# Kernel tuning notes

Measured on AMD Instinct MI355X. Metric: run time of the kernel, lower is better.

The kernel has to match this reference:

```python
import jax, jax.numpy as jnp
import numpy as np

HID = 100  # LSTM hidden size (fixed in module)


def _lstm_final(x, Wih, Whh, bih, bhh, reverse):
    # x: [N, T, Hin]; returns final hidden state [N, HID] (PyTorch gate order i,f,g,o)
    xs = jnp.flip(x, axis=1) if reverse else x
    pre = jnp.einsum('nth,gh->ntg', xs, Wih) + bih + bhh  # [N, T, 4*HID]
    N = x.shape[0]
    h0 = jnp.zeros((N, HID), x.dtype)
    c0 = jnp.zeros((N, HID), x.dtype)

    def step(carry, pt):
        h, c = carry
        g = pt + h @ Whh.T
        i, f, gg, o = jnp.split(g, 4, axis=-1)
        c = jax.nn.sigmoid(f) * c + jax.nn.sigmoid(i) * jnp.tanh(gg)
        h = jax.nn.sigmoid(o) * jnp.tanh(c)
        return (h, c), None

    (h, c), _ = jax.lax.scan(step, (h0, c0), jnp.swapaxes(pre, 0, 1))
    return h


def setup_inputs():
    key = jax.random.key(0)
    ks = jax.random.split(key, 16)
    H, B, S, NP, PL = 768, 40, 128, 100, 20
    w = lambda k, shape: jax.random.normal(k, shape, jnp.float32) * 0.02
    return {
        'bert_output': jax.random.normal(ks[0], (B, S, H), jnp.float32),
        'commonsense': jax.random.normal(ks[1], (B * NP, PL, H), jnp.float32),
        'attention_mask': jnp.ones((B, S), jnp.int32),
        'commonsense_mask': jnp.ones((B, NP), jnp.int32),
        'b_size': 8, 'num_cand': 5, 'num_path': NP, 'path_len': PL,
        'lstm_Wih_f': w(ks[2], (4 * HID, H)), 'lstm_Whh_f': w(ks[3], (4 * HID, HID)),
        'lstm_bih_f': jnp.zeros((4 * HID,), jnp.float32), 'lstm_bhh_f': jnp.zeros((4 * HID,), jnp.float32),
        'lstm_Wih_b': w(ks[4], (4 * HID, H)), 'lstm_Whh_b': w(ks[5], (4 * HID, HID)),
        'lstm_bih_b': jnp.zeros((4 * HID,), jnp.float32), 'lstm_bhh_b': jnp.zeros((4 * HID,), jnp.float32),
        'proj_W': w(ks[6], (H, 2 * HID)), 'proj_b': jnp.zeros((H,), jnp.float32),
        'W1_w': w(ks[7], (1, H)), 'W1_b': jnp.zeros((1,), jnp.float32),
        'W2_w': w(ks[8], (1, H)), 'W2_b': jnp.zeros((1,), jnp.float32),
        'W3': w(ks[9], (1, 1, H)),
        'attp_W': w(ks[10], (H, 4 * H)), 'attp_b': jnp.zeros((H,), jnp.float32),
        'ln_w': jnp.ones((H,), jnp.float32), 'ln_b': jnp.zeros((H,), jnp.float32),
    }


def reference(bert_output, commonsense, attention_mask, commonsense_mask,
              b_size, num_cand, num_path, path_len,
              lstm_Wih_f, lstm_Whh_f, lstm_bih_f, lstm_bhh_f,
              lstm_Wih_b, lstm_Whh_b, lstm_bih_b, lstm_bhh_b,
              proj_W, proj_b, W1_w, W1_b, W2_w, W2_b, W3,
              attp_W, attp_b, ln_w, ln_b):
    Bc = b_size * num_cand
    # bidirectional LSTM over commonsense paths; only final hidden states are used
    h_f = _lstm_final(commonsense, lstm_Wih_f, lstm_Whh_f, lstm_bih_f, lstm_bhh_f, False)
    h_b = _lstm_final(commonsense, lstm_Wih_b, lstm_Whh_b, lstm_bih_b, lstm_bhh_b, True)
    enc = jnp.concatenate([h_f, h_b], axis=-1)               # [Bc*NP, 200]
    cs = jax.nn.relu(enc @ proj_W.T + proj_b).reshape(Bc, num_path, -1)  # [B, P, H]
    # trilinear BiDAF-style scores
    part1 = bert_output @ W1_w.T + W1_b                      # [B, S, 1]
    part2 = (cs @ W2_w.T + W2_b).transpose(0, 2, 1)          # [B, 1, P]
    part3 = jnp.einsum('bsh,bph->bsp', W3 * bert_output, cs)  # [B, S, P]
    mask_cs = (1.0 - commonsense_mask.astype(jnp.float32)) * -10000.0
    mask_dqa = (1.0 - attention_mask.astype(jnp.float32)) * -10000.0
    total = part1 + part2 + part3 + mask_cs[:, None, :] + mask_dqa[:, :, None]
    cs_att = jax.nn.softmax(total, axis=-1)                  # over paths
    weight_cs = jnp.einsum('bsp,bph->bsh', cs_att, cs)
    ctx_att = jax.nn.softmax(total, axis=1)                  # over context tokens
    probs = jnp.einsum('bsp,btp->bst', cs_att, ctx_att)      # [B, S, S]
    weighted_context = jnp.einsum('bst,bth->bsh', probs, bert_output)
    cat = jnp.concatenate([bert_output, weight_cs, bert_output * weight_cs,
                           bert_output * weighted_context], axis=-1)
    x = jax.nn.relu(cat @ attp_W.T + attp_b) + bert_output
    u = x.mean(-1, keepdims=True)
    s = ((x - u) ** 2).mean(-1, keepdims=True)
    return ln_w * ((x - u) / jnp.sqrt(s + 1e-12)) + ln_b
```

## Files before the change

kernel.cpp:

```cpp
#include <hip/hip_runtime.h>


typedef unsigned short ushort_t;
typedef unsigned int u32;
typedef __attribute__((ext_vector_type(8))) short short8;
typedef __attribute__((ext_vector_type(4))) float f32x4;
typedef __attribute__((address_space(1))) const u32 gu32;
typedef __attribute__((address_space(3))) u32 lu32;

__device__ __forceinline__ ushort_t f2bf(float f) {
  u32 x = __builtin_bit_cast(u32, f);
  u32 r = (x + 0x7fffu + ((x >> 16) & 1u)) >> 16;
  return (ushort_t)r;
}
__device__ __forceinline__ float bflo(u32 u) { return __builtin_bit_cast(float, u << 16); }
__device__ __forceinline__ float bfhi(u32 u) { return __builtin_bit_cast(float, u & 0xffff0000u); }
__device__ __forceinline__ u32 cvtpk(float lo, float hi) {
  u32 r;
  asm("v_cvt_pk_bf16_f32 %0, %1, %2" : "=v"(r) : "v"(lo), "v"(hi));
  return r;
}

__device__ __forceinline__ float sigm(float x) { return 1.f / (1.f + __expf(-x)); }
__device__ __forceinline__ float tanh_f(float x) { return 1.f - 2.f / (__expf(2.f * x) + 1.f); }


__global__ void prep_weights(const float* __restrict__ Wih_f, const float* __restrict__ Wih_b,
                             const float* __restrict__ Whh_f, const float* __restrict__ Whh_b,
                             const float* __restrict__ bih_f, const float* __restrict__ bhh_f,
                             const float* __restrict__ bih_b, const float* __restrict__ bhh_b,
                             const float* __restrict__ projW, const float* __restrict__ attpW,
                             ushort_t* __restrict__ wihcat, ushort_t* __restrict__ whhcat,
                             float* __restrict__ biascat, ushort_t* __restrict__ projw_bf,
                             ushort_t* __restrict__ attpw_bf) {
  const int TOT = 614400 + 102400 + 800 + 196608 + 2359296;
  for (int idx = blockIdx.x * 256 + threadIdx.x; idx < TOT; idx += gridDim.x * 256) {
    if (idx < 614400) {
      int g = idx / 768, k = idx % 768;
      float v = g < 400 ? Wih_f[g * 768 + k] : Wih_b[(g - 400) * 768 + k];
      wihcat[idx] = f2bf(v);
    } else if (idx < 716800) {
      int e = idx - 614400; int g = e / 128, j = e % 128;
      float v = 0.f;
      if (j < 100) v = g < 400 ? Whh_f[g * 100 + j] : Whh_b[(g - 400) * 100 + j];
      whhcat[e] = f2bf(v);
    } else if (idx < 717600) {
      int g = idx - 716800;
      biascat[g] = g < 400 ? bih_f[g] + bhh_f[g] : bih_b[g - 400] + bhh_b[g - 400];
    } else if (idx < 914208) {
      int e = idx - 717600; int o = e / 256, j = e % 256;
      float v = 0.f;
      if (j < 100) v = projW[o * 200 + j];
      else if (j >= 128 && j < 228) v = projW[o * 200 + 100 + (j - 128)];
      projw_bf[e] = f2bf(v);
    } else {
      int e = idx - 914208;
      attpw_bf[e] = f2bf(attpW[e]);
    }
  }
}

__global__ __launch_bounds__(256) void prep_bert(const float* __restrict__ bert,
                                                 const float* __restrict__ W3,
                                                 ushort_t* __restrict__ bw3,
                                                 ushort_t* __restrict__ bT) {
  __shared__ ushort_t tl[64 * 130];
  int ht = blockIdx.x, b = blockIdx.y;
  int h0 = ht * 64, tid = threadIdx.x;
  for (int e = tid; e < 8192; e += 256) {
    int t = e >> 6, hh = e & 63;
    float v = bert[((size_t)b * 128 + t) * 768 + h0 + hh];
    bw3[((size_t)b * 128 + t) * 768 + h0 + hh] = f2bf(v * W3[h0 + hh]);
    tl[hh * 130 + t] = f2bf(v);
  }
  __syncthreads();
  for (int e = tid; e < 8192; e += 256) {
    int hh = e >> 7, t = e & 127;
    bT[((size_t)b * 768 + h0 + hh) * 128 + t] = tl[hh * 130 + t];
  }
}

__global__ __launch_bounds__(256) void csT_k(const ushort_t* __restrict__ csb,
                                             ushort_t* __restrict__ csT) {
  __shared__ ushort_t tl[64 * 130];
  int ht = blockIdx.x, b = blockIdx.y;
  int h0 = ht * 64, tid = threadIdx.x;
  for (int e = tid; e < 6400; e += 256) {
    int p = e >> 6, hh = e & 63;
    tl[hh * 130 + p] = csb[((size_t)b * 100 + p) * 768 + h0 + hh];
  }
  __syncthreads();
  for (int e = tid; e < 8192; e += 256) {
    int hh = e >> 7, p = e & 127;
    csT[((size_t)b * 768 + h0 + hh) * 128 + p] = (p < 100) ? tl[hh * 130 + p] : (ushort_t)0;
  }
}


__global__ __launch_bounds__(256) void gemm_pre_f(
    const float* __restrict__ X,
    const ushort_t* __restrict__ B,
    const float* __restrict__ bias,
    ushort_t* __restrict__ P)
{
  __shared__ __align__(16) float lsA[128 * 64];
  __shared__ __align__(16) ushort_t lsB[128 * 64];
  int bid = blockIdx.x;
  int xcd = bid & 7, slot = bid >> 3;
  int L = (xcd < 7) ? xcd * 547 + slot : 3829 + slot;
  int bm = L / 7, bn = L - bm * 7;
  int m0 = bm * 128, n0 = bn * 128;
  int tid = threadIdx.x, lane = tid & 63, w = tid >> 6;
  int wr = w >> 1, wc = w & 1;
  int l15 = lane & 15, lk = lane >> 4;
  f32x4 acc[4][4];
  #pragma unroll
  for (int i = 0; i < 4; ++i)
    #pragma unroll
    for (int j = 0; j < 4; ++j)
      #pragma unroll
      for (int r = 0; r < 4; ++r) acc[i][j][r] = 0.f;

  size_t abase[8];
  #pragma unroll
  for (int i = 0; i < 8; ++i) {
    int seg = w * 8 + i;
    int row = seg * 4 + (lane >> 4);
    int m = m0 + row;
    int t = m / 4000, sq = m - t * 4000;
    int lc = (lane & 15) ^ (row & 15);
    abase[i] = ((size_t)sq * 20 + t) * 768 + lc * 4;
  }
  int r_in = lane >> 3, pslot = lane & 7;

  for (int kt = 0; kt < 12; ++kt) {
    __syncthreads();
    #pragma unroll
    for (int i = 0; i < 8; ++i) {
      int seg = w * 8 + i;
      __builtin_amdgcn_global_load_lds(
          (gu32*)(X + abase[i] + kt * 64),
          (lu32*)((char*)lsA + seg * 1024), 16, 0, 0);
    }
    #pragma unroll
    for (int i = 0; i < 4; ++i) {
      int seg = w * 4 + i;
      int row = seg * 8 + r_in;
      int sl = pslot ^ (row & 7);
      int n = n0 + row;
      if (n < 800)
        __builtin_amdgcn_global_load_lds(
            (gu32*)(B + (size_t)n * 768 + kt * 64 + sl * 8),
            (lu32*)(lsB + seg * 512), 16, 0, 0);
    }
    __syncthreads();
    #pragma unroll
    for (int ks = 0; ks < 2; ++ks) {
      short8 af[4], bfv[4];
      #pragma unroll
      for (int f = 0; f < 4; ++f) {
        int row = wr * 64 + f * 16 + l15;
        int c0 = ks * 8 + lk * 2;
        int pc0 = c0 ^ (row & 15), pc1 = (c0 + 1) ^ (row & 15);
        float4 v0 = *reinterpret_cast<const float4*>(&lsA[row * 64 + pc0 * 4]);
        float4 v1 = *reinterpret_cast<const float4*>(&lsA[row * 64 + pc1 * 4]);
        int4 pk;
        pk.x = (int)cvtpk(v0.x, v0.y);
        pk.y = (int)cvtpk(v0.z, v0.w);
        pk.z = (int)cvtpk(v1.x, v1.y);
        pk.w = (int)cvtpk(v1.z, v1.w);
        af[f] = __builtin_bit_cast(short8, pk);
        int rowb = wc * 64 + f * 16 + l15;
        bfv[f] = *reinterpret_cast<const short8*>(
            &lsB[rowb * 64 + (((ks * 4 + lk) ^ (rowb & 7)) << 3)]);
      }
      #pragma unroll
      for (int fm = 0; fm < 4; ++fm)
        #pragma unroll
        for (int fn = 0; fn < 4; ++fn)
          acc[fm][fn] = __builtin_amdgcn_mfma_f32_16x16x32_bf16(af[fm], bfv[fn], acc[fm][fn], 0, 0, 0);
    }
  }
  #pragma unroll
  for (int fm = 0; fm < 4; ++fm) {
    int mb = m0 + wr * 64 + fm * 16;
    int t = mb / 4000;
    int sq = mb - t * 4000;
    int cch = sq >> 4;
    #pragma unroll
    for (int fn = 0; fn < 4; ++fn) {
      int nb = n0 + wc * 64 + fn * 16;
      if (nb < 800) {
        int nl = nb < 400 ? nb : nb - 400;
        int nq = (nb < 400 ? 0 : 25) + (nl >> 4);
        float bsv = bias[nb + l15];
        uint2 pk;
        pk.x = cvtpk(acc[fm][fn][0] + bsv, acc[fm][fn][1] + bsv);
        pk.y = cvtpk(acc[fm][fn][2] + bsv, acc[fm][fn][3] + bsv);
        *reinterpret_cast<uint2*>(
            &P[((((size_t)t * 250 + cch) * 50 + nq) << 8) + l15 * 16 + lk * 4]) = pk;
      }
    }
  }
}


template <int EPI>
__global__ __launch_bounds__(256) void gemm128(
    const ushort_t* __restrict__ A, int lda,
    const ushort_t* __restrict__ B, int ldb,
    int M, int N, int KT,
    const float* __restrict__ bias,
    const float* __restrict__ resid,
    float* __restrict__ C, int ldc,
    ushort_t* __restrict__ C2,
    int nbn, int swq, int swr)
{
  __shared__ __align__(16) ushort_t lsA[128 * 64];
  __shared__ __align__(16) ushort_t lsB[128 * 64];
  int bm, bn;
  if (nbn > 0) {
    int bid = blockIdx.x, xcd = bid & 7, slot = bid >> 3;
    int L = (xcd < swr) ? xcd * (swq + 1) + slot
                        : swr * (swq + 1) + (xcd - swr) * swq + slot;
    bm = L / nbn; bn = L - bm * nbn;
  } else {
    bm = blockIdx.x; bn = blockIdx.y;
  }
  int m0 = bm * 128, n0 = bn * 128;
  int tid = threadIdx.x, lane = tid & 63, w = tid >> 6;
  int wr = w >> 1, wc = w & 1;
  int l15 = lane & 15, lk = lane >> 4;
  f32x4 acc[4][4];
  #pragma unroll
  for (int i = 0; i < 4; ++i)
    #pragma unroll
    for (int j = 0; j < 4; ++j)
      #pragma unroll
      for (int r = 0; r < 4; ++r) acc[i][j][r] = 0.f;

  int r_in = lane >> 3, p = lane & 7;
  for (int kt = 0; kt < KT; ++kt) {
    __syncthreads();
    #pragma unroll
    for (int i = 0; i < 4; ++i) {
      int seg = w * 4 + i;
      int row = seg * 8 + r_in;
      int sl = p ^ (row & 7);
      int m = m0 + row;
      if (m < M)
        __builtin_amdgcn_global_load_lds(
            (gu32*)(A + (size_t)m * lda + kt * 64 + sl * 8),
            (lu32*)(lsA + seg * 512), 16, 0, 0);
      int n = n0 + row;
      if (n < N)
        __builtin_amdgcn_global_load_lds(
            (gu32*)(B + (size_t)n * ldb + kt * 64 + sl * 8),
            (lu32*)(lsB + seg * 512), 16, 0, 0);
    }
    __syncthreads();
    #pragma unroll
    for (int ks = 0; ks < 2; ++ks) {
      short8 af[4], bfv[4];
      #pragma unroll
      for (int f = 0; f < 4; ++f) {
        int row = wr * 64 + f * 16 + l15;
        af[f] = *reinterpret_cast<const short8*>(
            &lsA[row * 64 + (((ks * 4 + lk) ^ (row & 7)) << 3)]);
        int rowb = wc * 64 + f * 16 + l15;
        bfv[f] = *reinterpret_cast<const short8*>(
            &lsB[rowb * 64 + (((ks * 4 + lk) ^ (rowb & 7)) << 3)]);
      }
      #pragma unroll
      for (int fm = 0; fm < 4; ++fm)
        #pragma unroll
        for (int fn = 0; fn < 4; ++fn)
          acc[fm][fn] = __builtin_amdgcn_mfma_f32_16x16x32_bf16(af[fm], bfv[fn], acc[fm][fn], 0, 0, 0);
    }
  }
  #pragma unroll
  for (int fm = 0; fm < 4; ++fm)
    #pragma unroll
    for (int fn = 0; fn < 4; ++fn)
      #pragma unroll
      for (int r = 0; r < 4; ++r) {
        int m = m0 + wr * 64 + fm * 16 + lk * 4 + r;
        int n = n0 + wc * 64 + fn * 16 + l15;
        if (m < M && n < N) {
          float v = acc[fm][fn][r] + bias[n];
          v = fmaxf(v, 0.f);
          if (EPI == 2) v += resid[(size_t)m * ldc + n];
          C[(size_t)m * ldc + n] = v;
          if (EPI == 1 && C2) C2[(size_t)m * ldc + n] = f2bf(v);
        }
      }
}


template <int EPI>
__global__ __launch_bounds__(256) void gemm128b(
    const ushort_t* __restrict__ A, long long sA, int lda,
    const ushort_t* __restrict__ Bm, long long sB, int ldb,
    int M, int N, int KT,
    float* __restrict__ Cf, ushort_t* __restrict__ Cb, long long sC, int ldc,
    const float* __restrict__ p1, const float* __restrict__ p2,
    const int* __restrict__ am, const int* __restrict__ cm)
{
  __shared__ __align__(16) ushort_t lsA[128 * 64];
  __shared__ __align__(16) ushort_t lsB[128 * 64];
  int b = blockIdx.z;
  const ushort_t* Ab = A + (size_t)b * sA;
  const ushort_t* Bb = Bm + (size_t)b * sB;
  int n0 = blockIdx.x * 128;
  int tid = threadIdx.x, lane = tid & 63, w = tid >> 6;
  int wr = w >> 1, wc = w & 1;
  int l15 = lane & 15, lk = lane >> 4;
  f32x4 acc[4][4];
  #pragma unroll
  for (int i = 0; i < 4; ++i)
    #pragma unroll
    for (int j = 0; j < 4; ++j)
      #pragma unroll
      for (int r = 0; r < 4; ++r) acc[i][j][r] = 0.f;

  int r_in = lane >> 3, p = lane & 7;
  for (int kt = 0; kt < KT; ++kt) {
    __syncthreads();
    #pragma unroll
    for (int i = 0; i < 4; ++i) {
      int seg = w * 4 + i;
      int row = seg * 8 + r_in;
      int sl = p ^ (row & 7);
      if (row < M)
        __builtin_amdgcn_global_load_lds(
            (gu32*)(Ab + (size_t)row * lda + kt * 64 + sl * 8),
            (lu32*)(lsA + seg * 512), 16, 0, 0);
      int n = n0 + row;
      if (n < N)
        __builtin_amdgcn_global_load_lds(
            (gu32*)(Bb + (size_t)n * ldb + kt * 64 + sl * 8),
            (lu32*)(lsB + seg * 512), 16, 0, 0);
    }
    __syncthreads();
    #pragma unroll
    for (int ks = 0; ks < 2; ++ks) {
      short8 af[4], bfv[4];
      #pragma unroll
      for (int f = 0; f < 4; ++f) {
        int row = wr * 64 + f * 16 + l15;
        af[f] = *reinterpret_cast<const short8*>(
            &lsA[row * 64 + (((ks * 4 + lk) ^ (row & 7)) << 3)]);
        int rowb = wc * 64 + f * 16 + l15;
        bfv[f] = *reinterpret_cast<const short8*>(
            &lsB[rowb * 64 + (((ks * 4 + lk) ^ (rowb & 7)) << 3)]);
      }
      #pragma unroll
      for (int fm = 0; fm < 4; ++fm)
        #pragma unroll
        for (int fn = 0; fn < 4; ++fn)
          acc[fm][fn] = __builtin_amdgcn_mfma_f32_16x16x32_bf16(af[fm], bfv[fn], acc[fm][fn], 0, 0, 0);
    }
  }
  #pragma unroll
  for (int fm = 0; fm < 4; ++fm)
    #pragma unroll
    for (int fn = 0; fn < 4; ++fn)
      #pragma unroll
      for (int r = 0; r < 4; ++r) {
        int m = wr * 64 + fm * 16 + lk * 4 + r;
        int n = n0 + wc * 64 + fn * 16 + l15;
        if (m < M && n < N) {
          float v = acc[fm][fn][r];
          if (EPI == 10) {
            v += p1[b * M + m] + p2[b * N + n];
            v += (1.f - (float)am[b * M + m]) * -10000.f;
            v += (1.f - (float)cm[b * N + n]) * -10000.f;
            Cf[(size_t)b * sC + (size_t)m * ldc + n] = v;
          } else {
            Cb[(size_t)b * sC + (size_t)m * ldc + n] = f2bf(v);
          }
        }
      }
}


__global__ __launch_bounds__(256) void lstm_recur(
    const ushort_t* __restrict__ pre,
    const ushort_t* __restrict__ whh,
    ushort_t* __restrict__ hcat)
{
  __shared__ __align__(16) ushort_t gx[25 * 256];
  __shared__ __align__(16) ushort_t h_lds[16 * 128];

  int dir = blockIdx.y;
  int c = blockIdx.x;
  int tid = threadIdx.x, lane = tid & 63, w = tid >> 6;
  int s = lane & 15, lk = lane >> 4;

  short8 wf[7][4];
  #pragma unroll
  for (int qi = 0; qi < 7; ++qi) {
    int q = w + qi * 4;
    if (q < 25) {
      const ushort_t* wp = whh + ((size_t)dir * 400 + q * 16 + s) * 128;
      #pragma unroll
      for (int ks = 0; ks < 4; ++ks)
        wf[qi][ks] = *reinterpret_cast<const short8*>(wp + ks * 32 + lk * 8);
    }
  }
  for (int e = tid; e < 1024; e += 256)
    *reinterpret_cast<u32*>(&h_lds[e * 2]) = 0u;

  float cst[2][4];
  #pragma unroll
  for (int g = 0; g < 2; ++g)
    #pragma unroll
    for (int r = 0; r < 4; ++r) cst[g][r] = 0.f;

  uint2 pvA[7], pvB[7];
  {
    int tt0 = dir ? 19 : 0;
    const ushort_t* pb = pre + ((((size_t)tt0 * 250 + c) * 50 + dir * 25) << 8);
    #pragma unroll
    for (int qi = 0; qi < 7; ++qi) {
      int q = w + qi * 4;
      if (q < 25) pvA[qi] = *reinterpret_cast<const uint2*>(pb + (q << 8) + s * 16 + lk * 4);
    }
  }
  __syncthreads();

  auto step = [&](uint2 (&pvc)[7], uint2 (&pvn)[7], int t) {
    f32x4 acc[7];
    #pragma unroll
    for (int qi = 0; qi < 7; ++qi)
      #pragma unroll
      for (int r = 0; r < 4; ++r) acc[qi][r] = 0.f;
    #pragma unroll
    for (int ks = 0; ks < 4; ++ks) {
      short8 af = *reinterpret_cast<const short8*>(
          &h_lds[s * 128 + (((ks * 4 + lk) ^ s) << 3)]);
      #pragma unroll
      for (int qi = 0; qi < 7; ++qi)
        if (w + qi * 4 < 25)
          acc[qi] = __builtin_amdgcn_mfma_f32_16x16x32_bf16(af, wf[qi][ks], acc[qi], 0, 0, 0);
    }
    #pragma unroll
    for (int qi = 0; qi < 7; ++qi)
      if (w + qi * 4 < 25) {
        acc[qi][0] += bflo(pvc[qi].x); acc[qi][1] += bfhi(pvc[qi].x);
        acc[qi][2] += bflo(pvc[qi].y); acc[qi][3] += bfhi(pvc[qi].y);
      }
    if (t + 1 < 20) {
      int tn = dir ? 19 - (t + 1) : (t + 1);
      const ushort_t* pb = pre + ((((size_t)tn * 250 + c) * 50 + dir * 25) << 8);
      #pragma unroll
      for (int qi = 0; qi < 7; ++qi) {
        int q = w + qi * 4;
        if (q < 25) pvn[qi] = *reinterpret_cast<const uint2*>(pb + (q << 8) + s * 16 + lk * 4);
      }
    }
    #pragma unroll
    for (int qi = 0; qi < 7; ++qi) {
      int q = w + qi * 4;
      if (q < 25) {
        ushort4 pk;
        pk.x = f2bf(acc[qi][0]); pk.y = f2bf(acc[qi][1]);
        pk.z = f2bf(acc[qi][2]); pk.w = f2bf(acc[qi][3]);
        *reinterpret_cast<ushort4*>(&gx[(q << 8) + s * 16 + lk * 4]) = pk;
      }
    }
    __syncthreads();
    #pragma unroll
    for (int gd = 0; gd < 2; ++gd) {
      int gi = w + gd * 4;
      if (gi < 7) {
        int j = gi * 16 + s;
        if (j < 100) {
          auto ld2 = [&](int q, int sp) {
            return *reinterpret_cast<const uint2*>(&gx[(q << 8) + sp * 16 + lk * 4]);
          };
          uint2 iv = ld2(gi, s);
          uint2 fv = (s < 12) ? ld2(6 + gi, s + 4) : ld2(7 + gi, s - 12);
          uint2 gv = (s < 8) ? ld2(12 + gi, s + 8) : ld2(13 + gi, s - 8);
          uint2 ov = (s < 4) ? ld2(18 + gi, s + 12) : ld2(19 + gi, s - 4);
          float ia[4] = {bflo(iv.x), bfhi(iv.x), bflo(iv.y), bfhi(iv.y)};
          float fa[4] = {bflo(fv.x), bfhi(fv.x), bflo(fv.y), bfhi(fv.y)};
          float ga[4] = {bflo(gv.x), bfhi(gv.x), bflo(gv.y), bfhi(gv.y)};
          float oa[4] = {bflo(ov.x), bfhi(ov.x), bflo(ov.y), bfhi(ov.y)};
          #pragma unroll
          for (int r = 0; r < 4; ++r) {
            float cc = sigm(fa[r]) * cst[gd][r] + sigm(ia[r]) * tanh_f(ga[r]);
            cst[gd][r] = cc;
            int row = lk * 4 + r;
            h_lds[row * 128 + (((j >> 3) ^ row) << 3) + (j & 7)] =
                f2bf(sigm(oa[r]) * tanh_f(cc));
          }
        }
      }
    }
    __syncthreads();
  };

  #pragma unroll 1
  for (int tp = 0; tp < 10; ++tp) {
    step(pvA, pvB, 2 * tp);
    step(pvB, pvA, 2 * tp + 1);
  }

  {
    int row = tid >> 4, sl = tid & 15;
    uint2 v = *reinterpret_cast<const uint2*>(&h_lds[row * 128 + ((sl ^ row) << 3)]);
    *reinterpret_cast<uint2*>(&hcat[(size_t)(c * 16 + row) * 256 + dir * 128 + sl * 8]) = v;
  }
}


__global__ void rowdot2(const float* __restrict__ bert, const float* __restrict__ cs,
                        const float* __restrict__ W1w, const float* __restrict__ W1b,
                        const float* __restrict__ W2w, const float* __restrict__ W2b,
                        float* __restrict__ part1, float* __restrict__ part2) {
  int row = blockIdx.x;
  int lane = threadIdx.x;
  const float* x;
  const float* wv;
  float b0;
  float* out;
  if (row < 5120) { x = bert + (size_t)row * 768; wv = W1w; b0 = W1b[0]; out = part1 + row; }
  else { int r = row - 5120; x = cs + (size_t)r * 768; wv = W2w; b0 = W2b[0]; out = part2 + r; }
  float s = 0.f;
  for (int k = lane; k < 768; k += 64) s += x[k] * wv[k];
  for (int off = 32; off; off >>= 1) s += __shfl_down(s, off);
  if (lane == 0) *out = s + b0;
}

__global__ void softmax_both(const float* __restrict__ total,
                             ushort_t* __restrict__ csatt,
                             ushort_t* __restrict__ ctxatt) {
  int bid = blockIdx.x;
  int lane = threadIdx.x;
  if (bid < 5120) {
    const float* x = total + (size_t)bid * 100;
    float e0 = x[lane];
    bool has1 = (lane + 64) < 100;
    float e1 = has1 ? x[lane + 64] : -3.4e38f;
    float m = fmaxf(e0, e1);
    for (int off = 32; off; off >>= 1) m = fmaxf(m, __shfl_xor(m, off));
    float s0 = expf(e0 - m), s1 = has1 ? expf(e1 - m) : 0.f;
    float s = s0 + s1;
    for (int off = 32; off; off >>= 1) s += __shfl_xor(s, off);
    float inv = 1.f / s;
    csatt[(size_t)bid * 128 + lane] = f2bf(s0 * inv);
    csatt[(size_t)bid * 128 + lane + 64] = has1 ? f2bf(s1 * inv) : (ushort_t)0;
  } else {
    int idx = bid - 5120;
    int b = idx / 100, p = idx - b * 100;
    const float* base = total + (size_t)b * 12800 + p;
    float e0 = base[lane * 100], e1 = base[(lane + 64) * 100];
    float m = fmaxf(e0, e1);
    for (int off = 32; off; off >>= 1) m = fmaxf(m, __shfl_xor(m, off));
    float s0 = expf(e0 - m), s1 = expf(e1 - m);
    float s = s0 + s1;
    for (int off = 32; off; off >>= 1) s += __shfl_xor(s, off);
    float inv = 1.f / s;
    ctxatt[((size_t)b * 128 + lane) * 128 + p] = f2bf(s0 * inv);
    ctxatt[((size_t)b * 128 + lane + 64) * 128 + p] = f2bf(s1 * inv);
  }
}

__global__ void catk(const float* __restrict__ bert, const ushort_t* __restrict__ wcs,
                     const ushort_t* __restrict__ wctx, ushort_t* __restrict__ cat) {
  const int TOT = 5120 * 192;
  for (int i = blockIdx.x * 256 + threadIdx.x; i < TOT; i += gridDim.x * 256) {
    int row = i / 192, h4 = i - row * 192;
    size_t e = (size_t)row * 768 + h4 * 4;
    float4 bv = *reinterpret_cast<const float4*>(bert + e);
    ushort4 wv = *reinterpret_cast<const ushort4*>(wcs + e);
    ushort4 cv = *reinterpret_cast<const ushort4*>(wctx + e);
    ushort_t* out = cat + (size_t)row * 3072 + h4 * 4;
    ushort4 s0, s2, s3;
    s0.x = f2bf(bv.x); s0.y = f2bf(bv.y); s0.z = f2bf(bv.z); s0.w = f2bf(bv.w);
    s2.x = f2bf(bv.x * bflo((u32)wv.x)); s2.y = f2bf(bv.y * bflo((u32)wv.y));
    s2.z = f2bf(bv.z * bflo((u32)wv.z)); s2.w = f2bf(bv.w * bflo((u32)wv.w));
    s3.x = f2bf(bv.x * bflo((u32)cv.x)); s3.y = f2bf(bv.y * bflo((u32)cv.y));
    s3.z = f2bf(bv.z * bflo((u32)cv.z)); s3.w = f2bf(bv.w * bflo((u32)cv.w));
    *reinterpret_cast<ushort4*>(out) = s0;
    *reinterpret_cast<ushort4*>(out + 768) = wv;
    *reinterpret_cast<ushort4*>(out + 1536) = s2;
    *reinterpret_cast<ushort4*>(out + 2304) = s3;
  }
}

__global__ __launch_bounds__(256) void layernorm(float* __restrict__ X,
                                                 const float* __restrict__ w,
                                                 const float* __restrict__ bta) {
  int row = blockIdx.x;
  float* x = X + (size_t)row * 768;
  int t = threadIdx.x;
  float v[3];
  float s = 0.f;
  #pragma unroll
  for (int i = 0; i < 3; ++i) { v[i] = x[t + 256 * i]; s += v[i]; }
  __shared__ float red[256];
  red[t] = s; __syncthreads();
  for (int off = 128; off; off >>= 1) { if (t < off) red[t] += red[t + off]; __syncthreads(); }
  float mean = red[0] * (1.f / 768.f);
  __syncthreads();
  float q = 0.f;
  #pragma unroll
  for (int i = 0; i < 3; ++i) { float d = v[i] - mean; q += d * d; }
  red[t] = q; __syncthreads();
  for (int off = 128; off; off >>= 1) { if (t < off) red[t] += red[t + off]; __syncthreads(); }
  float inv = rsqrtf(red[0] * (1.f / 768.f) + 1e-12f);
  #pragma unroll
  for (int i = 0; i < 3; ++i) {
    int k = t + 256 * i;
    x[k] = w[k] * ((v[i] - mean) * inv) + bta[k];
  }
}


extern "C" void kernel_launch(void* const* d_in, const int* in_sizes, int n_in,
                              void* d_out, int out_size, void* d_ws, size_t ws_size,
                              hipStream_t stream) {
  (void)in_sizes; (void)n_in; (void)out_size; (void)ws_size;
  const float* bert  = (const float*)d_in[0];
  const float* cmn   = (const float*)d_in[1];
  const int*   amask = (const int*)d_in[2];
  const int*   cmask = (const int*)d_in[3];
  const float* Wih_f = (const float*)d_in[8];
  const float* Whh_f = (const float*)d_in[9];
  const float* bih_f = (const float*)d_in[10];
  const float* bhh_f = (const float*)d_in[11];
  const float* Wih_b = (const float*)d_in[12];
  const float* Whh_b = (const float*)d_in[13];
  const float* bih_b = (const float*)d_in[14];
  const float* bhh_b = (const float*)d_in[15];
  const float* projW = (const float*)d_in[16];
  const float* projb = (const float*)d_in[17];
  const float* W1w   = (const float*)d_in[18];
  const float* W1b   = (const float*)d_in[19];
  const float* W2w   = (const float*)d_in[20];
  const float* W2b   = (const float*)d_in[21];
  const float* W3    = (const float*)d_in[22];
  const float* attpW = (const float*)d_in[23];
  const float* attpb = (const float*)d_in[24];
  const float* lnw   = (const float*)d_in[25];
  const float* lnb   = (const float*)d_in[26];

  char* base = (char*)d_ws;
  size_t off = 0;
  auto alloc = [&](size_t bytes) -> char* {
    char* r = base + off;
    off += (bytes + 255) & ~(size_t)255;
    return r;
  };
  ushort_t* wihcat   = (ushort_t*)alloc(800 * 768 * 2);
  ushort_t* whhcat   = (ushort_t*)alloc(800 * 128 * 2);
  float*    biascat  = (float*)alloc(800 * 4);
  ushort_t* projw_bf = (ushort_t*)alloc(768 * 256 * 2);
  ushort_t* attpw_bf = (ushort_t*)alloc(768 * 3072 * 2);
  ushort_t* hcat     = (ushort_t*)alloc(4000 * 256 * 2);
  float*    cs       = (float*)alloc((size_t)4000 * 768 * 4);
  ushort_t* cs_bf    = (ushort_t*)alloc((size_t)4000 * 768 * 2);
  ushort_t* csT      = (ushort_t*)alloc((size_t)40 * 768 * 128 * 2);
  float*    part1    = (float*)alloc(5120 * 4);
  float*    part2    = (float*)alloc(4000 * 4);
  float*    total_s  = (float*)alloc((size_t)40 * 128 * 100 * 4);
  ushort_t* csatt_bf = (ushort_t*)alloc((size_t)40 * 128 * 128 * 2);
  ushort_t* ctxatt_bf= (ushort_t*)alloc((size_t)40 * 128 * 128 * 2);
  ushort_t* probs_bf = (ushort_t*)alloc((size_t)40 * 128 * 128 * 2);
  ushort_t* wcs_bf   = (ushort_t*)alloc((size_t)40 * 128 * 768 * 2);
  ushort_t* wctx_bf  = (ushort_t*)alloc((size_t)40 * 128 * 768 * 2);
  ushort_t* bw3_bf   = (ushort_t*)alloc((size_t)40 * 128 * 768 * 2);
  ushort_t* bertT    = (ushort_t*)alloc((size_t)40 * 768 * 128 * 2);
  ushort_t* cat      = (ushort_t*)alloc((size_t)5120 * 3072 * 2);
  ushort_t* pre      = (ushort_t*)alloc((size_t)20 * 250 * 50 * 256 * 2);

  prep_weights<<<512, 256, 0, stream>>>(Wih_f, Wih_b, Whh_f, Whh_b, bih_f, bhh_f, bih_b, bhh_b,
                                        projW, attpW, wihcat, whhcat, biascat, projw_bf, attpw_bf);
  prep_bert<<<dim3(12, 40), 256, 0, stream>>>(bert, W3, bw3_bf, bertT);

  gemm_pre_f<<<4375, 256, 0, stream>>>(cmn, wihcat, biascat, pre);
  lstm_recur<<<dim3(250, 2), 256, 0, stream>>>(pre, whhcat, hcat);

  gemm128<1><<<dim3(32, 6), 256, 0, stream>>>(hcat, 256, projw_bf, 256, 4000, 768, 4,
                                              projb, nullptr, cs, 768, cs_bf, 0, 0, 0);
  csT_k<<<dim3(12, 40), 256, 0, stream>>>(cs_bf, csT);
  rowdot2<<<9120, 64, 0, stream>>>(bert, cs, W1w, W1b, W2w, W2b, part1, part2);

  gemm128b<10><<<dim3(1, 1, 40), 256, 0, stream>>>(
      bw3_bf, 98304LL, 768, cs_bf, 76800LL, 768, 128, 100, 12,
      total_s, nullptr, 12800LL, 100, part1, part2, amask, cmask);
  softmax_both<<<9120, 64, 0, stream>>>(total_s, csatt_bf, ctxatt_bf);
  gemm128b<11><<<dim3(6, 1, 40), 256, 0, stream>>>(
      csatt_bf, 16384LL, 128, csT, 98304LL, 128, 128, 768, 2,
      nullptr, wcs_bf, 98304LL, 768, nullptr, nullptr, nullptr, nullptr);
  gemm128b<11><<<dim3(1, 1, 40), 256, 0, stream>>>(
      csatt_bf, 16384LL, 128, ctxatt_bf, 16384LL, 128, 128, 128, 2,
      nullptr, probs_bf, 16384LL, 128, nullptr, nullptr, nullptr, nullptr);
  gemm128b<11><<<dim3(6, 1, 40), 256, 0, stream>>>(
      probs_bf, 16384LL, 128, bertT, 98304LL, 128, 128, 768, 2,
      nullptr, wctx_bf, 98304LL, 768, nullptr, nullptr, nullptr, nullptr);

  catk<<<2048, 256, 0, stream>>>(bert, wcs_bf, wctx_bf, cat);
  gemm128<2><<<240, 256, 0, stream>>>(cat, 3072, attpw_bf, 3072, 5120, 768, 48,
                                      attpb, bert, (float*)d_out, 768, nullptr, 6, 30, 0);
  layernorm<<<5120, 256, 0, stream>>>((float*)d_out, lnw, lnb);
}
```

Measured before the change: 535.4 us.

## Fuse attention GEMMs and concat epilogues, pre-convert LSTM input, retile GEMMs

The commonsense input is now converted to bf16 in time-major order by a separate kernel, so the input-projection GEMM reads bf16 through a 128x160 tile instead of converting fp32 in its inner loop. The score GEMM is split four ways along K, and the mask and part1/part2 additions move into the softmax, which sums the four partials. The cs-weighted and probs GEMMs are merged by placing the context-attention matrix next to csT, and their epilogues write straight into the concat buffer, so catk and two intermediate buffers go away. The final projection uses 64-row tiles to launch more blocks. The costs are an extra full pass writing bf16 x, and redundant partial-sum traffic in the softmax.

```diff
diff --git a/kernel.cpp b/kernel.cpp
--- a/kernel.cpp
+++ b/kernel.cpp
@@ -60,18 +60,34 @@
   }
 }
 
+__global__ void convert_x_t(const float4* __restrict__ x4, ushort_t* __restrict__ xb) {
+  for (int i = blockIdx.x * 256 + threadIdx.x; i < 15360000; i += gridDim.x * 256) {
+    int seq = i / 3840;
+    int rem = i - seq * 3840;
+    int t = rem / 192;
+    int k4 = rem - t * 192;
+    float4 v = x4[i];
+    ushort4 o;
+    o.x = f2bf(v.x); o.y = f2bf(v.y); o.z = f2bf(v.z); o.w = f2bf(v.w);
+    *reinterpret_cast<ushort4*>(&xb[((size_t)t * 4000 + seq) * 768 + k4 * 4]) = o;
+  }
+}
+
 __global__ __launch_bounds__(256) void prep_bert(const float* __restrict__ bert,
                                                  const float* __restrict__ W3,
                                                  ushort_t* __restrict__ bw3,
-                                                 ushort_t* __restrict__ bT) {
+                                                 ushort_t* __restrict__ bT,
+                                                 ushort_t* __restrict__ cat) {
   __shared__ ushort_t tl[64 * 130];
   int ht = blockIdx.x, b = blockIdx.y;
   int h0 = ht * 64, tid = threadIdx.x;
   for (int e = tid; e < 8192; e += 256) {
     int t = e >> 6, hh = e & 63;
     float v = bert[((size_t)b * 128 + t) * 768 + h0 + hh];
+    ushort_t vb = f2bf(v);
     bw3[((size_t)b * 128 + t) * 768 + h0 + hh] = f2bf(v * W3[h0 + hh]);
-    tl[hh * 130 + t] = f2bf(v);
+    cat[((size_t)b * 128 + t) * 3072 + h0 + hh] = vb;
+    tl[hh * 130 + t] = vb;
   }
   __syncthreads();
   for (int e = tid; e < 8192; e += 256) {
@@ -81,7 +97,7 @@
 }
 
 __global__ __launch_bounds__(256) void csT_k(const ushort_t* __restrict__ csb,
-                                             ushort_t* __restrict__ csT) {
+                                             ushort_t* __restrict__ csTcat) {
   __shared__ ushort_t tl[64 * 130];
   int ht = blockIdx.x, b = blockIdx.y;
   int h0 = ht * 64, tid = threadIdx.x;
@@ -92,92 +108,76 @@
   __syncthreads();
   for (int e = tid; e < 8192; e += 256) {
     int hh = e >> 7, p = e & 127;
-    csT[((size_t)b * 768 + h0 + hh) * 128 + p] = (p < 100) ? tl[hh * 130 + p] : (ushort_t)0;
-  }
-}
-
-
-__global__ __launch_bounds__(256) void gemm_pre_f(
-    const float* __restrict__ X,
+    csTcat[((size_t)b * 896 + h0 + hh) * 128 + p] = (p < 100) ? tl[hh * 130 + p] : (ushort_t)0;
+  }
+}
+
+
+__global__ __launch_bounds__(256) void gemm_pre160(
+    const ushort_t* __restrict__ A,
     const ushort_t* __restrict__ B,
     const float* __restrict__ bias,
     ushort_t* __restrict__ P)
 {
-  __shared__ __align__(16) float lsA[128 * 64];
-  __shared__ __align__(16) ushort_t lsB[128 * 64];
+  __shared__ __align__(16) ushort_t lsA[128 * 64];
+  __shared__ __align__(16) ushort_t lsB[160 * 64];
   int bid = blockIdx.x;
   int xcd = bid & 7, slot = bid >> 3;
-  int L = (xcd < 7) ? xcd * 547 + slot : 3829 + slot;
-  int bm = L / 7, bn = L - bm * 7;
-  int m0 = bm * 128, n0 = bn * 128;
+  int L = (xcd < 5) ? xcd * 391 + slot : 1955 + (xcd - 5) * 390 + slot;
+  int bm = L / 5, bn = L - bm * 5;
+  int m0 = bm * 128, n0 = bn * 160;
   int tid = threadIdx.x, lane = tid & 63, w = tid >> 6;
   int wr = w >> 1, wc = w & 1;
   int l15 = lane & 15, lk = lane >> 4;
-  f32x4 acc[4][4];
+  f32x4 acc[4][5];
   #pragma unroll
   for (int i = 0; i < 4; ++i)
     #pragma unroll
-    for (int j = 0; j < 4; ++j)
+    for (int j = 0; j < 5; ++j)
       #pragma unroll
       for (int r = 0; r < 4; ++r) acc[i][j][r] = 0.f;
 
-  size_t abase[8];
-  #pragma unroll
-  for (int i = 0; i < 8; ++i) {
-    int seg = w * 8 + i;
-    int row = seg * 4 + (lane >> 4);
-    int m = m0 + row;
-    int t = m / 4000, sq = m - t * 4000;
-    int lc = (lane & 15) ^ (row & 15);
-    abase[i] = ((size_t)sq * 20 + t) * 768 + lc * 4;
-  }
-  int r_in = lane >> 3, pslot = lane & 7;
-
+  int r_in = lane >> 3, p = lane & 7;
   for (int kt = 0; kt < 12; ++kt) {
     __syncthreads();
-    #pragma unroll
-    for (int i = 0; i < 8; ++i) {
-      int seg = w * 8 + i;
-      __builtin_amdgcn_global_load_lds(
-          (gu32*)(X + abase[i] + kt * 64),
-          (lu32*)((char*)lsA + seg * 1024), 16, 0, 0);
-    }
     #pragma unroll
     for (int i = 0; i < 4; ++i) {
       int seg = w * 4 + i;
       int row = seg * 8 + r_in;
-      int sl = pslot ^ (row & 7);
-      int n = n0 + row;
-      if (n < 800)
-        __builtin_amdgcn_global_load_lds(
-            (gu32*)(B + (size_t)n * 768 + kt * 64 + sl * 8),
-            (lu32*)(lsB + seg * 512), 16, 0, 0);
+      int sl = p ^ (row & 7);
+      __builtin_amdgcn_global_load_lds(
+          (gu32*)(A + (size_t)(m0 + row) * 768 + kt * 64 + sl * 8),
+          (lu32*)(lsA + seg * 512), 16, 0, 0);
+    }
+    #pragma unroll
+    for (int i = 0; i < 5; ++i) {
+      int seg = w * 5 + i;
+      int row = seg * 8 + r_in;
+      int sl = p ^ (row & 7);
+      __builtin_amdgcn_global_load_lds(
+          (gu32*)(B + (size_t)(n0 + row) * 768 + kt * 64 + sl * 8),
+          (lu32*)(lsB + seg * 512), 16, 0, 0);
     }
     __syncthreads();
     #pragma unroll
     for (int ks = 0; ks < 2; ++ks) {
-      short8 af[4], bfv[4];
+      short8 af[4], bfv[5];
       #pragma unroll
       for (int f = 0; f < 4; ++f) {
         int row = wr * 64 + f * 16 + l15;
-        int c0 = ks * 8 + lk * 2;
-        int pc0 = c0 ^ (row & 15), pc1 = (c0 + 1) ^ (row & 15);
-        float4 v0 = *reinterpret_cast<const float4*>(&lsA[row * 64 + pc0 * 4]);
-        float4 v1 = *reinterpret_cast<const float4*>(&lsA[row * 64 + pc1 * 4]);
-        int4 pk;
-        pk.x = (int)cvtpk(v0.x, v0.y);
-        pk.y = (int)cvtpk(v0.z, v0.w);
-        pk.z = (int)cvtpk(v1.x, v1.y);
-        pk.w = (int)cvtpk(v1.z, v1.w);
-        af[f] = __builtin_bit_cast(short8, pk);
-        int rowb = wc * 64 + f * 16 + l15;
+        af[f] = *reinterpret_cast<const short8*>(
+            &lsA[row * 64 + (((ks * 4 + lk) ^ (row & 7)) << 3)]);
+      }
+      #pragma unroll
+      for (int f = 0; f < 5; ++f) {
+        int rowb = wc * 80 + f * 16 + l15;
         bfv[f] = *reinterpret_cast<const short8*>(
             &lsB[rowb * 64 + (((ks * 4 + lk) ^ (rowb & 7)) << 3)]);
       }
       #pragma unroll
       for (int fm = 0; fm < 4; ++fm)
         #pragma unroll
-        for (int fn = 0; fn < 4; ++fn)
+        for (int fn = 0; fn < 5; ++fn)
           acc[fm][fn] = __builtin_amdgcn_mfma_f32_16x16x32_bf16(af[fm], bfv[fn], acc[fm][fn], 0, 0, 0);
     }
   }
@@ -188,45 +188,32 @@
     int sq = mb - t * 4000;
     int cch = sq >> 4;
     #pragma unroll
-    for (int fn = 0; fn < 4; ++fn) {
-      int nb = n0 + wc * 64 + fn * 16;
-      if (nb < 800) {
-        int nl = nb < 400 ? nb : nb - 400;
-        int nq = (nb < 400 ? 0 : 25) + (nl >> 4);
-        float bsv = bias[nb + l15];
-        uint2 pk;
-        pk.x = cvtpk(acc[fm][fn][0] + bsv, acc[fm][fn][1] + bsv);
-        pk.y = cvtpk(acc[fm][fn][2] + bsv, acc[fm][fn][3] + bsv);
-        *reinterpret_cast<uint2*>(
-            &P[((((size_t)t * 250 + cch) * 50 + nq) << 8) + l15 * 16 + lk * 4]) = pk;
-      }
-    }
-  }
-}
-
-
-template <int EPI>
-__global__ __launch_bounds__(256) void gemm128(
+    for (int fn = 0; fn < 5; ++fn) {
+      int nb = n0 + wc * 80 + fn * 16;
+      int nl = nb < 400 ? nb : nb - 400;
+      int nq = (nb < 400 ? 0 : 25) + (nl >> 4);
+      float bsv = bias[nb + l15];
+      uint2 pk;
+      pk.x = cvtpk(acc[fm][fn][0] + bsv, acc[fm][fn][1] + bsv);
+      pk.y = cvtpk(acc[fm][fn][2] + bsv, acc[fm][fn][3] + bsv);
+      *reinterpret_cast<uint2*>(
+          &P[((((size_t)t * 250 + cch) * 50 + nq) << 8) + l15 * 16 + lk * 4]) = pk;
+    }
+  }
+}
+
+
+__global__ __launch_bounds__(256) void gemm_proj(
     const ushort_t* __restrict__ A, int lda,
     const ushort_t* __restrict__ B, int ldb,
     int M, int N, int KT,
     const float* __restrict__ bias,
-    const float* __restrict__ resid,
     float* __restrict__ C, int ldc,
-    ushort_t* __restrict__ C2,
-    int nbn, int swq, int swr)
+    ushort_t* __restrict__ C2)
 {
   __shared__ __align__(16) ushort_t lsA[128 * 64];
   __shared__ __align__(16) ushort_t lsB[128 * 64];
-  int bm, bn;
-  if (nbn > 0) {
-    int bid = blockIdx.x, xcd = bid & 7, slot = bid >> 3;
-    int L = (xcd < swr) ? xcd * (swq + 1) + slot
-                        : swr * (swq + 1) + (xcd - swr) * swq + slot;
-    bm = L / nbn; bn = L - bm * nbn;
-  } else {
-    bm = blockIdx.x; bn = blockIdx.y;
-  }
+  int bm = blockIdx.x, bn = blockIdx.y;
   int m0 = bm * 128, n0 = bn * 128;
   int tid = threadIdx.x, lane = tid & 63, w = tid >> 6;
   int wr = w >> 1, wc = w & 1;
@@ -287,11 +274,9 @@
         int m = m0 + wr * 64 + fm * 16 + lk * 4 + r;
         int n = n0 + wc * 64 + fn * 16 + l15;
         if (m < M && n < N) {
-          float v = acc[fm][fn][r] + bias[n];
-          v = fmaxf(v, 0.f);
-          if (EPI == 2) v += resid[(size_t)m * ldc + n];
+          float v = fmaxf(acc[fm][fn][r] + bias[n], 0.f);
           C[(size_t)m * ldc + n] = v;
-          if (EPI == 1 && C2) C2[(size_t)m * ldc + n] = f2bf(v);
+          C2[(size_t)m * ldc + n] = f2bf(v);
         }
       }
 }
@@ -302,13 +287,13 @@
     const ushort_t* __restrict__ A, long long sA, int lda,
     const ushort_t* __restrict__ Bm, long long sB, int ldb,
     int M, int N, int KT,
-    float* __restrict__ Cf, ushort_t* __restrict__ Cb, long long sC, int ldc,
-    const float* __restrict__ p1, const float* __restrict__ p2,
-    const int* __restrict__ am, const int* __restrict__ cm)
+    float* __restrict__ Cf, ushort_t* __restrict__ Cb,
+    const float* __restrict__ bertp, ushort_t* __restrict__ catp)
 {
   __shared__ __align__(16) ushort_t lsA[128 * 64];
   __shared__ __align__(16) ushort_t lsB[128 * 64];
   int b = blockIdx.z;
+  int koff = blockIdx.y * KT * 64;
   const ushort_t* Ab = A + (size_t)b * sA;
   const ushort_t* Bb = Bm + (size_t)b * sB;
   int n0 = blockIdx.x * 128;
@@ -333,12 +318,12 @@
       int sl = p ^ (row & 7);
       if (row < M)
         __builtin_amdgcn_global_load_lds(
-            (gu32*)(Ab + (size_t)row * lda + kt * 64 + sl * 8),
+            (gu32*)(Ab + (size_t)row * lda + koff + kt * 64 + sl * 8),
             (lu32*)(lsA + seg * 512), 16, 0, 0);
       int n = n0 + row;
       if (n < N)
         __builtin_amdgcn_global_load_lds(
-            (gu32*)(Bb + (size_t)n * ldb + kt * 64 + sl * 8),
+            (gu32*)(Bb + (size_t)n * ldb + koff + kt * 64 + sl * 8),
             (lu32*)(lsB + seg * 512), 16, 0, 0);
     }
     __syncthreads();
@@ -372,14 +357,105 @@
         if (m < M && n < N) {
           float v = acc[fm][fn][r];
           if (EPI == 10) {
-            v += p1[b * M + m] + p2[b * N + n];
-            v += (1.f - (float)am[b * M + m]) * -10000.f;
-            v += (1.f - (float)cm[b * N + n]) * -10000.f;
-            Cf[(size_t)b * sC + (size_t)m * ldc + n] = v;
+            Cf[(size_t)blockIdx.y * 512000 + (size_t)b * 12800 + (size_t)m * 100 + n] = v;
+          } else if (EPI == 12) {
+            size_t row3 = ((size_t)b * 128 + m) * 3072;
+            if (n < 768) {
+              float bv = bertp[((size_t)b * 128 + m) * 768 + n];
+              ushort_t wv = f2bf(v);
+              catp[row3 + 768 + n] = wv;
+              catp[row3 + 1536 + n] = f2bf(bv * bflo((u32)wv));
+            } else {
+              Cb[(size_t)b * 16384 + (size_t)m * 128 + (n - 768)] = f2bf(v);
+            }
           } else {
-            Cb[(size_t)b * sC + (size_t)m * ldc + n] = f2bf(v);
+            float bv = bertp[((size_t)b * 128 + m) * 768 + n];
+            catp[((size_t)b * 128 + m) * 3072 + 2304 + n] = f2bf(bv * v);
           }
         }
+      }
+}
+
+
+__global__ __launch_bounds__(256) void gemm64_attp(
+    const ushort_t* __restrict__ A,
+    const ushort_t* __restrict__ B,
+    const float* __restrict__ bias,
+    const float* __restrict__ resid,
+    float* __restrict__ C)
+{
+  __shared__ __align__(16) ushort_t lsA[64 * 64];
+  __shared__ __align__(16) ushort_t lsB[128 * 64];
+  int bid = blockIdx.x;
+  int xcd = bid & 7, slot = bid >> 3;
+  int L = xcd * 60 + slot;
+  int bm = L / 6, bn = L - bm * 6;
+  int m0 = bm * 64, n0 = bn * 128;
+  int tid = threadIdx.x, lane = tid & 63, w = tid >> 6;
+  int wr = w >> 1, wc = w & 1;
+  int l15 = lane & 15, lk = lane >> 4;
+  f32x4 acc[2][4];
+  #pragma unroll
+  for (int i = 0; i < 2; ++i)
+    #pragma unroll
+    for (int j = 0; j < 4; ++j)
+      #pragma unroll
+      for (int r = 0; r < 4; ++r) acc[i][j][r] = 0.f;
+
+  int r_in = lane >> 3, p = lane & 7;
+  for (int kt = 0; kt < 48; ++kt) {
+    __syncthreads();
+    #pragma unroll
+    for (int i = 0; i < 2; ++i) {
+      int seg = w * 2 + i;
+      int row = seg * 8 + r_in;
+      int sl = p ^ (row & 7);
+      __builtin_amdgcn_global_load_lds(
+          (gu32*)(A + (size_t)(m0 + row) * 3072 + kt * 64 + sl * 8),
+          (lu32*)(lsA + seg * 512), 16, 0, 0);
+    }
+    #pragma unroll
+    for (int i = 0; i < 4; ++i) {
+      int seg = w * 4 + i;
+      int row = seg * 8 + r_in;
+      int sl = p ^ (row & 7);
+      __builtin_amdgcn_global_load_lds(
+          (gu32*)(B + (size_t)(n0 + row) * 3072 + kt * 64 + sl * 8),
+          (lu32*)(lsB + seg * 512), 16, 0, 0);
+    }
+    __syncthreads();
+    #pragma unroll
+    for (int ks = 0; ks < 2; ++ks) {
+      short8 af[2], bfv[4];
+      #pragma unroll
+      for (int f = 0; f < 2; ++f) {
+        int row = wr * 32 + f * 16 + l15;
+        af[f] = *reinterpret_cast<const short8*>(
+            &lsA[row * 64 + (((ks * 4 + lk) ^ (row & 7)) << 3)]);
+      }
+      #pragma unroll
+      for (int f = 0; f < 4; ++f) {
+        int rowb = wc * 64 + f * 16 + l15;
+        bfv[f] = *reinterpret_cast<const short8*>(
+            &lsB[rowb * 64 + (((ks * 4 + lk) ^ (rowb & 7)) << 3)]);
+      }
+      #pragma unroll
+      for (int fm = 0; fm < 2; ++fm)
+        #pragma unroll
+        for (int fn = 0; fn < 4; ++fn)
+          acc[fm][fn] = __builtin_amdgcn_mfma_f32_16x16x32_bf16(af[fm], bfv[fn], acc[fm][fn], 0, 0, 0);
+    }
+  }
+  #pragma unroll
+  for (int fm = 0; fm < 2; ++fm)
+    #pragma unroll
+    for (int fn = 0; fn < 4; ++fn)
+      #pragma unroll
+      for (int r = 0; r < 4; ++r) {
+        int m = m0 + wr * 32 + fm * 16 + lk * 4 + r;
+        int n = n0 + wc * 64 + fn * 16 + l15;
+        float v = fmaxf(acc[fm][fn][r] + bias[n], 0.f) + resid[(size_t)m * 768 + n];
+        C[(size_t)m * 768 + n] = v;
       }
 }
 
@@ -533,16 +609,28 @@
   if (lane == 0) *out = s + b0;
 }
 
-__global__ void softmax_both(const float* __restrict__ total,
+__global__ void softmax_both(const float* __restrict__ t4,
+                             const float* __restrict__ part1,
+                             const float* __restrict__ part2,
+                             const int* __restrict__ amask,
+                             const int* __restrict__ cmask,
                              ushort_t* __restrict__ csatt,
-                             ushort_t* __restrict__ ctxatt) {
+                             ushort_t* __restrict__ csTcat) {
   int bid = blockIdx.x;
   int lane = threadIdx.x;
+  auto tsum = [&](size_t idx) {
+    return t4[idx] + t4[idx + 512000] + t4[idx + 1024000] + t4[idx + 1536000];
+  };
   if (bid < 5120) {
-    const float* x = total + (size_t)bid * 100;
-    float e0 = x[lane];
+    int b = bid >> 7;
+    size_t base = (size_t)bid * 100;
+    float e0 = tsum(base + lane) + part2[b * 100 + lane]
+               + (1.f - (float)cmask[b * 100 + lane]) * -10000.f;
     bool has1 = (lane + 64) < 100;
-    float e1 = has1 ? x[lane + 64] : -3.4e38f;
+    float e1 = -3.4e38f;
+    if (has1)
+      e1 = tsum(base + lane + 64) + part2[b * 100 + lane + 64]
+           + (1.f - (float)cmask[b * 100 + lane + 64]) * -10000.f;
     float m = fmaxf(e0, e1);
     for (int off = 32; off; off >>= 1) m = fmaxf(m, __shfl_xor(m, off));
     float s0 = expf(e0 - m), s1 = has1 ? expf(e1 - m) : 0.f;
@@ -554,39 +642,20 @@
   } else {
     int idx = bid - 5120;
     int b = idx / 100, p = idx - b * 100;
-    const float* base = total + (size_t)b * 12800 + p;
-    float e0 = base[lane * 100], e1 = base[(lane + 64) * 100];
+    size_t base = (size_t)b * 12800 + p;
+    int t0 = lane, t1 = lane + 64;
+    float e0 = tsum(base + (size_t)t0 * 100) + part1[b * 128 + t0]
+               + (1.f - (float)amask[b * 128 + t0]) * -10000.f;
+    float e1 = tsum(base + (size_t)t1 * 100) + part1[b * 128 + t1]
+               + (1.f - (float)amask[b * 128 + t1]) * -10000.f;
     float m = fmaxf(e0, e1);
     for (int off = 32; off; off >>= 1) m = fmaxf(m, __shfl_xor(m, off));
     float s0 = expf(e0 - m), s1 = expf(e1 - m);
     float s = s0 + s1;
     for (int off = 32; off; off >>= 1) s += __shfl_xor(s, off);
     float inv = 1.f / s;
-    ctxatt[((size_t)b * 128 + lane) * 128 + p] = f2bf(s0 * inv);
-    ctxatt[((size_t)b * 128 + lane + 64) * 128 + p] = f2bf(s1 * inv);
-  }
-}
-
-__global__ void catk(const float* __restrict__ bert, const ushort_t* __restrict__ wcs,
-                     const ushort_t* __restrict__ wctx, ushort_t* __restrict__ cat) {
-  const int TOT = 5120 * 192;
-  for (int i = blockIdx.x * 256 + threadIdx.x; i < TOT; i += gridDim.x * 256) {
-    int row = i / 192, h4 = i - row * 192;
-    size_t e = (size_t)row * 768 + h4 * 4;
-    float4 bv = *reinterpret_cast<const float4*>(bert + e);
-    ushort4 wv = *reinterpret_cast<const ushort4*>(wcs + e);
-    ushort4 cv = *reinterpret_cast<const ushort4*>(wctx + e);
-    ushort_t* out = cat + (size_t)row * 3072 + h4 * 4;
-    ushort4 s0, s2, s3;
-    s0.x = f2bf(bv.x); s0.y = f2bf(bv.y); s0.z = f2bf(bv.z); s0.w = f2bf(bv.w);
-    s2.x = f2bf(bv.x * bflo((u32)wv.x)); s2.y = f2bf(bv.y * bflo((u32)wv.y));
-    s2.z = f2bf(bv.z * bflo((u32)wv.z)); s2.w = f2bf(bv.w * bflo((u32)wv.w));
-    s3.x = f2bf(bv.x * bflo((u32)cv.x)); s3.y = f2bf(bv.y * bflo((u32)cv.y));
-    s3.z = f2bf(bv.z * bflo((u32)cv.z)); s3.w = f2bf(bv.w * bflo((u32)cv.w));
-    *reinterpret_cast<ushort4*>(out) = s0;
-    *reinterpret_cast<ushort4*>(out + 768) = wv;
-    *reinterpret_cast<ushort4*>(out + 1536) = s2;
-    *reinterpret_cast<ushort4*>(out + 2304) = s3;
+    csTcat[((size_t)b * 896 + 768 + t0) * 128 + p] = f2bf(s0 * inv);
+    csTcat[((size_t)b * 896 + 768 + t1) * 128 + p] = f2bf(s1 * inv);
   }
 }
 
@@ -662,48 +731,43 @@
   ushort_t* hcat     = (ushort_t*)alloc(4000 * 256 * 2);
   float*    cs       = (float*)alloc((size_t)4000 * 768 * 4);
   ushort_t* cs_bf    = (ushort_t*)alloc((size_t)4000 * 768 * 2);
-  ushort_t* csT      = (ushort_t*)alloc((size_t)40 * 768 * 128 * 2);
+  ushort_t* csTcat   = (ushort_t*)alloc((size_t)40 * 896 * 128 * 2);
   float*    part1    = (float*)alloc(5120 * 4);
   float*    part2    = (float*)alloc(4000 * 4);
-  float*    total_s  = (float*)alloc((size_t)40 * 128 * 100 * 4);
+  float*    total4   = (float*)alloc((size_t)4 * 40 * 128 * 100 * 4);
   ushort_t* csatt_bf = (ushort_t*)alloc((size_t)40 * 128 * 128 * 2);
-  ushort_t* ctxatt_bf= (ushort_t*)alloc((size_t)40 * 128 * 128 * 2);
   ushort_t* probs_bf = (ushort_t*)alloc((size_t)40 * 128 * 128 * 2);
-  ushort_t* wcs_bf   = (ushort_t*)alloc((size_t)40 * 128 * 768 * 2);
-  ushort_t* wctx_bf  = (ushort_t*)alloc((size_t)40 * 128 * 768 * 2);
   ushort_t* bw3_bf   = (ushort_t*)alloc((size_t)40 * 128 * 768 * 2);
   ushort_t* bertT    = (ushort_t*)alloc((size_t)40 * 768 * 128 * 2);
   ushort_t* cat      = (ushort_t*)alloc((size_t)5120 * 3072 * 2);
+  ushort_t* x_bf     = (ushort_t*)alloc((size_t)20 * 4000 * 768 * 2);
   ushort_t* pre      = (ushort_t*)alloc((size_t)20 * 250 * 50 * 256 * 2);
 
   prep_weights<<<512, 256, 0, stream>>>(Wih_f, Wih_b, Whh_f, Whh_b, bih_f, bhh_f, bih_b, bhh_b,
                                         projW, attpW, wihcat, whhcat, biascat, projw_bf, attpw_bf);
-  prep_bert<<<dim3(12, 40), 256, 0, stream>>>(bert, W3, bw3_bf, bertT);
-
-  gemm_pre_f<<<4375, 256, 0, stream>>>(cmn, wihcat, biascat, pre);
+  prep_bert<<<dim3(12, 40), 256, 0, stream>>>(bert, W3, bw3_bf, bertT, cat);
+  convert_x_t<<<2048, 256, 0, stream>>>((const float4*)cmn, x_bf);
+
+  gemm_pre160<<<3125, 256, 0, stream>>>(x_bf, wihcat, biascat, pre);
   lstm_recur<<<dim3(250, 2), 256, 0, stream>>>(pre, whhcat, hcat);
 
-  gemm128<1><<<dim3(32, 6), 256, 0, stream>>>(hcat, 256, projw_bf, 256, 4000, 768, 4,
-                                              projb, nullptr, cs, 768, cs_bf, 0, 0, 0);
-  csT_k<<<dim3(12, 40), 256, 0, stream>>>(cs_bf, csT);
+  gemm_proj<<<dim3(32, 6), 256, 0, stream>>>(hcat, 256, projw_bf, 256, 4000, 768, 4,
+                                             projb, cs, 768, cs_bf);
+  csT_k<<<dim3(12, 40), 256, 0, stream>>>(cs_bf, csTcat);
   rowdot2<<<9120, 64, 0, stream>>>(bert, cs, W1w, W1b, W2w, W2b, part1, part2);
 
-  gemm128b<10><<<dim3(1, 1, 40), 256, 0, stream>>>(
-      bw3_bf, 98304LL, 768, cs_bf, 76800LL, 768, 128, 100, 12,
-      total_s, nullptr, 12800LL, 100, part1, part2, amask, cmask);
-  softmax_both<<<9120, 64, 0, stream>>>(total_s, csatt_bf, ctxatt_bf);
-  gemm128b<11><<<dim3(6, 1, 40), 256, 0, stream>>>(
-      csatt_bf, 16384LL, 128, csT, 98304LL, 128, 128, 768, 2,
-      nullptr, wcs_bf, 98304LL, 768, nullptr, nullptr, nullptr, nullptr);
-  gemm128b<11><<<dim3(1, 1, 40), 256, 0, stream>>>(
-      csatt_bf, 16384LL, 128, ctxatt_bf, 16384LL, 128, 128, 128, 2,
-      nullptr, probs_bf, 16384LL, 128, nullptr, nullptr, nullptr, nullptr);
-  gemm128b<11><<<dim3(6, 1, 40), 256, 0, stream>>>(
+  gemm128b<10><<<dim3(1, 4, 40), 256, 0, stream>>>(
+      bw3_bf, 98304LL, 768, cs_bf, 76800LL, 768, 128, 100, 3,
+      total4, nullptr, nullptr, nullptr);
+  softmax_both<<<9120, 64, 0, stream>>>(total4, part1, part2, amask, cmask,
+                                        csatt_bf, csTcat);
+  gemm128b<12><<<dim3(7, 1, 40), 256, 0, stream>>>(
+      csatt_bf, 16384LL, 128, csTcat, 114688LL, 128, 128, 896, 2,
+      nullptr, probs_bf, bert, cat);
+  gemm128b<13><<<dim3(6, 1, 40), 256, 0, stream>>>(
       probs_bf, 16384LL, 128, bertT, 98304LL, 128, 128, 768, 2,
-      nullptr, wctx_bf, 98304LL, 768, nullptr, nullptr, nullptr, nullptr);
-
-  catk<<<2048, 256, 0, stream>>>(bert, wcs_bf, wctx_bf, cat);
-  gemm128<2><<<240, 256, 0, stream>>>(cat, 3072, attpw_bf, 3072, 5120, 768, 48,
-                                      attpb, bert, (float*)d_out, 768, nullptr, 6, 30, 0);
+      nullptr, nullptr, bert, cat);
+
+  gemm64_attp<<<480, 256, 0, stream>>>(cat, attpw_bf, attpb, bert, (float*)d_out);
   layernorm<<<5120, 256, 0, stream>>>((float*)d_out, lnw, lnb);
 }
```

New measurement: 497.4 us. -7.1%, faster.
